# Kernel tuning notes

Measured on AMD Instinct MI355X. Metric: run time of the kernel, lower is better.

Reference implementation:

```python
import jax, jax.numpy as jnp
import numpy as np

NUM_EXPERTS = 8
TOP_K = 2
HIDDEN = 2048
INTER = 7168
B, S = 4, 2048


def setup_inputs() -> dict:
    key = jax.random.key(0)
    k0, k1, k2, k3, k4 = jax.random.split(key, 5)
    scale_h = 1.0 / np.sqrt(HIDDEN)
    scale_i = 1.0 / np.sqrt(INTER)
    return {
        "hidden_states": jax.random.normal(k0, (B, S, HIDDEN), dtype=jnp.float32),
        "gate_w": jax.random.normal(k1, (NUM_EXPERTS, HIDDEN), dtype=jnp.float32) * scale_h,
        "w1": jax.random.normal(k2, (NUM_EXPERTS, INTER, HIDDEN), dtype=jnp.float32) * scale_h,
        "w3": jax.random.normal(k3, (NUM_EXPERTS, INTER, HIDDEN), dtype=jnp.float32) * scale_h,
        "w2": jax.random.normal(k4, (NUM_EXPERTS, HIDDEN, INTER), dtype=jnp.float32) * scale_i,
    }


def reference(hidden_states, gate_w, w1, w3, w2):
    orig_shape = hidden_states.shape
    x = hidden_states.reshape(-1, HIDDEN)              # [T, H]

    # Router: gate linear -> softmax -> top-k -> renormalize.
    router_logits = x @ gate_w.T                       # [T, E]
    probs = jax.nn.softmax(router_logits, axis=-1)
    topk_w, topk_idx = jax.lax.top_k(probs, TOP_K)     # [T, K]
    topk_w = topk_w / jnp.sum(topk_w, axis=-1, keepdims=True)

    # Dense combine weights: [T, E] with top-k renormalized weights scattered.
    combine = jnp.sum(
        jax.nn.one_hot(topk_idx, NUM_EXPERTS, dtype=x.dtype) * topk_w[..., None],
        axis=1,
    )                                                   # [T, E]

    out = jnp.zeros_like(x)
    # Fixed small loop over experts (structurally distinct weight matrices);
    # avoids materializing a [T, E, I] intermediate.
    for e in range(NUM_EXPERTS):
        g = jax.nn.silu(x @ w1[e].T)                   # [T, I]
        u = x @ w3[e].T                                # [T, I]
        y = (g * u) @ w2[e].T                          # [T, H]
        out = out + combine[:, e:e + 1] * y

    return out.reshape(orig_shape)
```

## Files before the change

### kernel.cpp

```cpp
#include <hip/hip_runtime.h>
#include <stdint.h>

#define NE    8
#define HID   2048
#define INTER 7168
#define TTOK  8192
#define NT1   (HID / 64)
#define NT2   (INTER / 64)

typedef __bf16 bf16;
typedef bf16 bf16x4 __attribute__((ext_vector_type(4)));
typedef bf16 bf16x8 __attribute__((ext_vector_type(8)));
typedef float f32x4 __attribute__((ext_vector_type(4)));

__device__ __forceinline__ void glds16(const void* g, void* l) {
  __builtin_amdgcn_global_load_lds((__attribute__((address_space(1))) void*)g,
                                   (__attribute__((address_space(3))) void*)l, 16, 0, 0);
}

__global__ void cvt_f32_bf16(const float* __restrict__ src, bf16* __restrict__ dst, long n) {
  long i = (long)blockIdx.x * blockDim.x + threadIdx.x;
  long stride = (long)gridDim.x * blockDim.x;
  for (long j = i * 4; j < n; j += stride * 4) {
    float4 v = *(const float4*)(src + j);
    bf16x4 o = {(bf16)v.x, (bf16)v.y, (bf16)v.z, (bf16)v.w};
    *(bf16x4*)(dst + j) = o;
  }
}

__global__ void router_kernel(const float* __restrict__ x, const float* __restrict__ gw,
                              int* __restrict__ topk_e, float* __restrict__ topk_w) {
  const int wid = threadIdx.x >> 6, lane = threadIdx.x & 63;
  const int t = blockIdx.x * 4 + wid;
  if (t >= TTOK) return;
  const float* xr = x + (size_t)t * HID;
  float xv[32];
#pragma unroll
  for (int i = 0; i < 32; ++i) xv[i] = xr[lane + 64 * i];
  float lg[NE];
#pragma unroll
  for (int e = 0; e < NE; ++e) {
    const float* g = gw + e * HID;
    float s = 0.f;
#pragma unroll
    for (int i = 0; i < 32; ++i) s += xv[i] * g[lane + 64 * i];
#pragma unroll
    for (int off = 32; off; off >>= 1) s += __shfl_down(s, off);
    lg[e] = s;
  }
  if (lane == 0) {
    int i1 = 0;
#pragma unroll
    for (int e = 1; e < NE; ++e) if (lg[e] > lg[i1]) i1 = e;
    int i2 = (i1 == 0) ? 1 : 0;
#pragma unroll
    for (int e = 0; e < NE; ++e) if (e != i2 && e != i1 && lg[e] > lg[i2]) i2 = e;
    float r = __expf(lg[i2] - lg[i1]);
    float wa = 1.f / (1.f + r);
    topk_e[2 * t] = i1; topk_e[2 * t + 1] = i2;
    topk_w[2 * t] = wa; topk_w[2 * t + 1] = 1.f - wa;
  }
}

__global__ void gather_sorted(const int* __restrict__ topk_e, const float* __restrict__ topk_w,
                              int* __restrict__ cnt, int* __restrict__ ltok,
                              float* __restrict__ lw, int* __restrict__ ppos) {
  const int e = blockIdx.x;
  const int tid = threadIdx.x;
  const int lane = tid & 63, wv = tid >> 6;
  __shared__ int wtot[4];
  __shared__ int basesh;
  if (tid == 0) basesh = 0;
  __syncthreads();
  for (int c0 = 0; c0 < TTOK; c0 += 256) {
    const int t = c0 + tid;
    const int e0 = topk_e[2 * t], e1 = topk_e[2 * t + 1];
    const int j = (e0 == e) ? 0 : 1;
    const int flag = (e0 == e) || (e1 == e);
    unsigned long long b = __ballot(flag);
    int wrank = __popcll(b & ((1ULL << lane) - 1ULL));
    if (lane == 63) wtot[wv] = __popcll(b);
    __syncthreads();
    int wbase = 0;
#pragma unroll
    for (int k = 0; k < 4; ++k) if (k < wv) wbase += wtot[k];
    const int total = wtot[0] + wtot[1] + wtot[2] + wtot[3];
    const int pos = basesh + wbase + wrank;
    if (flag) {
      ltok[e * TTOK + pos] = t;
      lw[e * TTOK + pos] = (j == 0) ? topk_w[2 * t] : topk_w[2 * t + 1];
      ppos[2 * t + j] = pos;
    }
    __syncthreads();
    if (tid == 0) basesh += total;
    __syncthreads();
  }
  if (tid == 0) cnt[e] = basesh;
}

__global__ void prefix_kernel(const int* __restrict__ cnt, int* __restrict__ base) {
  if (threadIdx.x == 0 && blockIdx.x == 0) {
    int b = 0;
    for (int e = 0; e < NE; ++e) { base[e] = b; b += cnt[e]; }
    base[NE] = b;
  }
}

__global__ void combine_kernel(const float* __restrict__ ybuf, const int* __restrict__ topk_e,
                               const int* __restrict__ ppos, const int* __restrict__ basep,
                               float* __restrict__ out) {
  const int t = blockIdx.x;
  const int col = threadIdx.x * 8;
  const int g0 = basep[topk_e[2 * t]] + ppos[2 * t];
  const int g1 = basep[topk_e[2 * t + 1]] + ppos[2 * t + 1];
  const float4* y0 = (const float4*)(ybuf + (size_t)g0 * HID + col);
  const float4* y1 = (const float4*)(ybuf + (size_t)g1 * HID + col);
  float4* o = (float4*)(out + (size_t)t * HID + col);
  float4 a0 = y0[0], b0 = y1[0];
  float4 a1 = y0[1], b1 = y1[1];
  o[0] = make_float4(a0.x + b0.x, a0.y + b0.y, a0.z + b0.z, a0.w + b0.w);
  o[1] = make_float4(a1.x + b1.x, a1.y + b1.y, a1.z + b1.z, a1.w + b1.w);
}


#define MFMA(a, b, c) __builtin_amdgcn_mfma_f32_16x16x32_bf16((a), (b), (c), 0, 0, 0)

#define STAGE_A(h, kt) do { int _b = ((kt) & 1) * 32768; size_t _k = (size_t)(kt) * 128; \
    glds16(bA + oA[(h)*2 + 0] + _k, ldsA + _b + (h) * 16384 + d0); \
    glds16(bA + oA[(h)*2 + 1] + _k, ldsA + _b + (h) * 16384 + d1); } while (0)
#define STAGE_B(h, kt) do { int _b = ((kt) & 1) * 32768; size_t _k = (size_t)(kt) * 128; \
    glds16(bB + oB[(h)*2 + 0] + _k, ldsB + _b + (h) * 16384 + d0); \
    glds16(bB + oB[(h)*2 + 1] + _k, ldsB + _b + (h) * 16384 + d1); } while (0)

#define RD_A(mf, ks) (*(const bf16x8*)(ldsA + curb + arow + (mf) * (16 * 128) + ((ks) ? kcol1 : kcol0)))
#define RD_B(nf, ks) (*(const bf16x8*)(ldsB + curb + brow + (nf) * (16 * 128) + ((ks) ? kcol1 : kcol0)))

#define BAR()    __builtin_amdgcn_s_barrier()
#define LGKMC(n) do { asm volatile("s_waitcnt lgkmcnt(" #n ")" ::: "memory"); \
                      __builtin_amdgcn_sched_barrier(0); } while (0)
#define SCHED0() __builtin_amdgcn_sched_barrier(0)

#define Q_MFMA(AM, BM, ACCM, ACCN_OFF) do { \
  __builtin_amdgcn_s_setprio(1); \
  _Pragma("unroll") \
  for (int m = 0; m < 4; ++m) \
    _Pragma("unroll") \
    for (int n = 0; n < 2; ++n) { \
      acc[ACCM + m][ACCN_OFF + n] = MFMA(AM[m][0], BM[n][0], acc[ACCM + m][ACCN_OFF + n]); \
      acc[ACCM + m][ACCN_OFF + n] = MFMA(AM[m][1], BM[n][1], acc[ACCM + m][ACCN_OFF + n]); \
    } \
  __builtin_amdgcn_s_setprio(0); \
} while (0)

__launch_bounds__(512, 2)
__global__ void pass1_kernel(const bf16* __restrict__ xb, const bf16* __restrict__ w1b,
                             bf16* __restrict__ hbuf, const int* __restrict__ cnt,
                             const int* __restrict__ basep, const int* __restrict__ ltok) {
  const int e = blockIdx.z;
  const int c = cnt[e];
  const int tm = blockIdx.y;
  if (tm * 256 >= c) return;
  const int tn = blockIdx.x;

  __shared__ __align__(16) bf16 sA[2][256 * 64];
  __shared__ __align__(16) bf16 sB[2][256 * 64];
  char* const ldsA = (char*)&sA[0][0];
  char* const ldsB = (char*)&sB[0][0];

  const int tid = threadIdx.x;
  const int r0 = tid >> 3;
  const int ls = (tid & 7) ^ (r0 & 7);
  const int d0 = tid * 16, d1 = (tid + 512) * 16;
  const char* const bA = (const char*)xb;
  const char* const bB = (const char*)w1b;

  uint32_t oA[4], oB[4];
#pragma unroll
  for (int i = 0; i < 4; ++i) {
    int trow = i * 64 + r0;
    int slot = tm * 256 + trow; if (slot >= c) slot = c - 1;
    oA[i] = (uint32_t)((size_t)ltok[e * TTOK + slot] * (HID * 2) + ls * 16);
    int br = i * 64 + r0;
    int w = (br >> 4) & 1;
    int wr = tn * 128 + ((br >> 5) << 4) + (br & 15);
    size_t off = ((size_t)e * INTER + wr) * (HID * 2) + (size_t)ls * 16;
    if (w) off += (size_t)NE * INTER * HID * 2;
    oB[i] = (uint32_t)off;
  }

  const int lane = tid & 63, wid = tid >> 6;
  const int wm = wid >> 2, wn = wid & 3;
  const int ln15 = lane & 15, kq = lane >> 4;
  const int swz = (ln15 & 7) << 4;
  const int kcol0 = (kq * 16) ^ swz;
  const int kcol1 = (64 + kq * 16) ^ swz;
  const int arow = (wm * 128 + ln15) * 128;
  const int brow = (wn * 64 + ln15) * 128;

  f32x4 acc[8][4];
#pragma unroll
  for (int m = 0; m < 8; ++m)
#pragma unroll
    for (int n = 0; n < 4; ++n) acc[m][n] = (f32x4){0.f, 0.f, 0.f, 0.f};

  STAGE_A(0, 0); STAGE_A(1, 0); STAGE_B(0, 0); STAGE_B(1, 0);
  asm volatile("s_waitcnt vmcnt(4)" ::: "memory");
  STAGE_A(0, 1); STAGE_A(1, 1); STAGE_B(0, 1);
  asm volatile("s_waitcnt vmcnt(6)" ::: "memory");
  BAR();

  bf16x8 a0[4][2], a1[4][2], b0[2][2], b1[2][2];
  int cur = 0;
  for (int t = 0; t < NT1; ++t, cur ^= 1) {
    const int curb = cur * 32768;
#pragma unroll
    for (int m = 0; m < 4; ++m) { a0[m][0] = RD_A(m, 0); a0[m][1] = RD_A(m, 1); }
#pragma unroll
    for (int n = 0; n < 2; ++n) { b0[n][0] = RD_B(n, 0); b0[n][1] = RD_B(n, 1); }
    if (t + 1 < NT1) STAGE_B(1, t + 1);
    BAR(); LGKMC(12);
    if (t > 0) Q_MFMA(a1, b1, 4, 2);
    BAR();
#pragma unroll
    for (int m = 0; m < 4; ++m) { a1[m][0] = RD_A(4 + m, 0); a1[m][1] = RD_A(4 + m, 1); }
    BAR(); LGKMC(8);
    Q_MFMA(a0, b0, 0, 0);
    BAR();
#pragma unroll
    for (int n = 0; n < 2; ++n) { b1[n][0] = RD_B(2 + n, 0); b1[n][1] = RD_B(2 + n, 1); }
    if (t + 2 < NT1) { STAGE_A(0, t + 2); STAGE_A(1, t + 2); SCHED0(); }
    BAR(); LGKMC(4);
    Q_MFMA(a1, b0, 4, 0);
    BAR();
    if (t + 2 < NT1) STAGE_B(0, t + 2);
    LGKMC(0);
    Q_MFMA(a0, b1, 0, 2);
    if (t + 2 < NT1) asm volatile("s_waitcnt vmcnt(6)" ::: "memory");
    else             asm volatile("s_waitcnt vmcnt(0)" ::: "memory");
    BAR();
  }
  Q_MFMA(a1, b1, 4, 2);

  const int be = basep[e];
#pragma unroll
  for (int mh = 0; mh < 2; ++mh)
#pragma unroll
    for (int mf = 0; mf < 4; ++mf)
#pragma unroll
      for (int j = 0; j < 4; ++j) {
        const int slot = tm * 256 + wm * 128 + mh * 64 + mf * 16 + kq * 4 + j;
        if (slot < c) {
          bf16* hrow = hbuf + (size_t)(be + slot) * INTER + tn * 128;
#pragma unroll
          for (int p = 0; p < 2; ++p) {
            const float g = acc[mh * 4 + mf][2 * p][j];
            const float u = acc[mh * 4 + mf][2 * p + 1][j];
            const float hv = g / (1.f + __expf(-g)) * u;
            hrow[wn * 32 + p * 16 + ln15] = (bf16)hv;
          }
        }
      }
}

__launch_bounds__(512, 2)
__global__ void pass2_kernel(const bf16* __restrict__ hbuf, const bf16* __restrict__ w2b,
                             float* __restrict__ ybuf, const int* __restrict__ cnt,
                             const int* __restrict__ basep, const float* __restrict__ lw) {
  const int e = blockIdx.z;
  const int c = cnt[e];
  const int tm = blockIdx.y;
  if (tm * 256 >= c) return;
  const int tn = blockIdx.x;

  __shared__ __align__(16) bf16 sA[2][256 * 64];
  __shared__ __align__(16) bf16 sB[2][256 * 64];
  char* const ldsA = (char*)&sA[0][0];
  char* const ldsB = (char*)&sB[0][0];

  const int tid = threadIdx.x;
  const int r0 = tid >> 3;
  const int ls = (tid & 7) ^ (r0 & 7);
  const int d0 = tid * 16, d1 = (tid + 512) * 16;
  const int be = basep[e];
  const char* const bA = (const char*)hbuf;
  const char* const bB = (const char*)w2b;

  uint32_t oA[4], oB[4];
#pragma unroll
  for (int i = 0; i < 4; ++i) {
    int trow = i * 64 + r0;
    int slot = tm * 256 + trow; if (slot >= c) slot = c - 1;
    oA[i] = (uint32_t)((size_t)(be + slot) * (INTER * 2) + ls * 16);
    oB[i] = (uint32_t)(((size_t)e * HID + tn * 256 + i * 64 + r0) * (INTER * 2) + (size_t)ls * 16);
  }

  const int lane = tid & 63, wid = tid >> 6;
  const int wm = wid >> 2, wn = wid & 3;
  const int ln15 = lane & 15, kq = lane >> 4;
  const int swz = (ln15 & 7) << 4;
  const int kcol0 = (kq * 16) ^ swz;
  const int kcol1 = (64 + kq * 16) ^ swz;
  const int arow = (wm * 128 + ln15) * 128;
  const int brow = (wn * 64 + ln15) * 128;

  f32x4 acc[8][4];
#pragma unroll
  for (int m = 0; m < 8; ++m)
#pragma unroll
    for (int n = 0; n < 4; ++n) acc[m][n] = (f32x4){0.f, 0.f, 0.f, 0.f};

  STAGE_A(0, 0); STAGE_A(1, 0); STAGE_B(0, 0); STAGE_B(1, 0);
  asm volatile("s_waitcnt vmcnt(4)" ::: "memory");
  STAGE_A(0, 1); STAGE_A(1, 1); STAGE_B(0, 1);
  asm volatile("s_waitcnt vmcnt(6)" ::: "memory");
  BAR();

  bf16x8 a0[4][2], a1[4][2], b0[2][2], b1[2][2];
  int cur = 0;
  for (int t = 0; t < NT2; ++t, cur ^= 1) {
    const int curb = cur * 32768;
#pragma unroll
    for (int m = 0; m < 4; ++m) { a0[m][0] = RD_A(m, 0); a0[m][1] = RD_A(m, 1); }
#pragma unroll
    for (int n = 0; n < 2; ++n) { b0[n][0] = RD_B(n, 0); b0[n][1] = RD_B(n, 1); }
    if (t + 1 < NT2) STAGE_B(1, t + 1);
    BAR(); LGKMC(12);
    if (t > 0) Q_MFMA(a1, b1, 4, 2);
    BAR();
#pragma unroll
    for (int m = 0; m < 4; ++m) { a1[m][0] = RD_A(4 + m, 0); a1[m][1] = RD_A(4 + m, 1); }
    BAR(); LGKMC(8);
    Q_MFMA(a0, b0, 0, 0);
    BAR();
#pragma unroll
    for (int n = 0; n < 2; ++n) { b1[n][0] = RD_B(2 + n, 0); b1[n][1] = RD_B(2 + n, 1); }
    if (t + 2 < NT2) { STAGE_A(0, t + 2); STAGE_A(1, t + 2); SCHED0(); }
    BAR(); LGKMC(4);
    Q_MFMA(a1, b0, 4, 0);
    BAR();
    if (t + 2 < NT2) STAGE_B(0, t + 2);
    LGKMC(0);
    Q_MFMA(a0, b1, 0, 2);
    if (t + 2 < NT2) asm volatile("s_waitcnt vmcnt(6)" ::: "memory");
    else             asm volatile("s_waitcnt vmcnt(0)" ::: "memory");
    BAR();
  }
  Q_MFMA(a1, b1, 4, 2);

#pragma unroll
  for (int mh = 0; mh < 2; ++mh)
#pragma unroll
    for (int mf = 0; mf < 4; ++mf)
#pragma unroll
      for (int j = 0; j < 4; ++j) {
        const int slot = tm * 256 + wm * 128 + mh * 64 + mf * 16 + kq * 4 + j;
        if (slot < c) {
          const float wt = lw[e * TTOK + slot];
          float* yrow = ybuf + (size_t)(be + slot) * HID + tn * 256;
#pragma unroll
          for (int n = 0; n < 4; ++n)
            yrow[wn * 64 + n * 16 + ln15] = wt * acc[mh * 4 + mf][n][j];
        }
      }
}

extern "C" void kernel_launch(void* const* d_in, const int* in_sizes, int n_in,
                              void* d_out, int out_size, void* d_ws, size_t ws_size,
                              hipStream_t stream) {
  const float* x  = (const float*)d_in[0];
  const float* gw = (const float*)d_in[1];
  const float* w1 = (const float*)d_in[2];
  const float* w3 = (const float*)d_in[3];
  const float* w2 = (const float*)d_in[4];
  float* out = (float*)d_out;

  char* ws = (char*)d_ws;
  size_t off = 0;
  auto take = [&](size_t bytes) -> char* {
    char* p = ws + off;
    off += (bytes + 255) & ~(size_t)255;
    return p;
  };
  bf16* xb    = (bf16*)take((size_t)TTOK * HID * 2);
  bf16* w1b   = (bf16*)take((size_t)NE * INTER * HID * 2);
  bf16* w3b   = (bf16*)take((size_t)NE * INTER * HID * 2);
  bf16* w2b   = (bf16*)take((size_t)NE * HID * INTER * 2);
  bf16* hbuf  = (bf16*)take((size_t)TTOK * 2 * INTER * 2);
  float* ybuf = (float*)take((size_t)TTOK * 2 * HID * 4);
  int*   topk_e = (int*)take(TTOK * 2 * 4);
  float* topk_w = (float*)take(TTOK * 2 * 4);
  int*   ltok   = (int*)take(NE * TTOK * 4);
  float* lwgt   = (float*)take(NE * TTOK * 4);
  int*   ppos   = (int*)take(TTOK * 2 * 4);
  int*   cntp   = (int*)take(64);
  int*   basep  = (int*)take(64);
  if (off > ws_size) return;

  cvt_f32_bf16<<<2048, 256, 0, stream>>>(x,  xb,  (long)TTOK * HID);
  cvt_f32_bf16<<<4096, 256, 0, stream>>>(w1, w1b, (long)NE * INTER * HID);
  cvt_f32_bf16<<<4096, 256, 0, stream>>>(w3, w3b, (long)NE * INTER * HID);
  cvt_f32_bf16<<<4096, 256, 0, stream>>>(w2, w2b, (long)NE * HID * INTER);

  router_kernel<<<TTOK / 4, 256, 0, stream>>>(x, gw, topk_e, topk_w);
  gather_sorted<<<NE, 256, 0, stream>>>(topk_e, topk_w, cntp, ltok, lwgt, ppos);
  prefix_kernel<<<1, 64, 0, stream>>>(cntp, basep);

  pass1_kernel<<<dim3(INTER / 128, TTOK / 256, NE), 512, 0, stream>>>(
      xb, w1b, hbuf, cntp, basep, ltok);
  pass2_kernel<<<dim3(HID / 256, TTOK / 256, NE), 512, 0, stream>>>(
      hbuf, w2b, ybuf, cntp, basep, lwgt);
  combine_kernel<<<TTOK, 256, 0, stream>>>(ybuf, topk_e, ppos, basep, out);
}
```

Baseline: 2.103 ms.

## Fuse fp32-to-bf16 weight conversion into GEMM B-tile loads

Removes the three separate weight conversion kernels and has pass1/pass2 load fp32 weights straight into registers, convert them to bf16 and write them to LDS. This drops the full-size bf16 weight write and re-read (about 1.4 GB of fp32 read plus bf16 write/read). In exchange, each GEMM tile now re-reads fp32 weights, twice the bytes per load, and does so once per token tile, with register staging in place of async direct-to-LDS loads. That can add global traffic and register pressure in the main loop.

```diff
diff --git a/kernel.cpp b/kernel.cpp
--- a/kernel.cpp
+++ b/kernel.cpp
@@ -16,6 +16,13 @@
 __device__ __forceinline__ void glds16(const void* g, void* l) {
   __builtin_amdgcn_global_load_lds((__attribute__((address_space(1))) void*)g,
                                    (__attribute__((address_space(3))) void*)l, 16, 0, 0);
+}
+
+__device__ __forceinline__ bf16x8 cvt8(float4 lo, float4 hi) {
+  bf16x8 v;
+  v[0] = (bf16)lo.x; v[1] = (bf16)lo.y; v[2] = (bf16)lo.z; v[3] = (bf16)lo.w;
+  v[4] = (bf16)hi.x; v[5] = (bf16)hi.y; v[6] = (bf16)hi.z; v[7] = (bf16)hi.w;
+  return v;
 }
 
 __global__ void cvt_f32_bf16(const float* __restrict__ src, bf16* __restrict__ dst, long n) {
@@ -128,9 +135,19 @@
 #define STAGE_A(h, kt) do { int _b = ((kt) & 1) * 32768; size_t _k = (size_t)(kt) * 128; \
     glds16(bA + oA[(h)*2 + 0] + _k, ldsA + _b + (h) * 16384 + d0); \
     glds16(bA + oA[(h)*2 + 1] + _k, ldsA + _b + (h) * 16384 + d1); } while (0)
-#define STAGE_B(h, kt) do { int _b = ((kt) & 1) * 32768; size_t _k = (size_t)(kt) * 128; \
-    glds16(bB + oB[(h)*2 + 0] + _k, ldsB + _b + (h) * 16384 + d0); \
-    glds16(bB + oB[(h)*2 + 1] + _k, ldsB + _b + (h) * 16384 + d1); } while (0)
+
+#define BLOAD(kt) do { size_t _k = (size_t)(kt) * 256; \
+    _Pragma("unroll") \
+    for (int i = 0; i < 4; ++i) { \
+      bl[i][0] = *(const float4*)(pB + oBf[i] + _k); \
+      bl[i][1] = *(const float4*)(pB + oBf[i] + _k + 16); \
+    } } while (0)
+
+#define BWRITE(kt) do { int _nb = ((kt) & 1) * 32768; \
+    _Pragma("unroll") \
+    for (int i = 0; i < 4; ++i) { \
+      *(bf16x8*)(ldsB + _nb + (i >> 1) * 16384 + ((i & 1) ? d1 : d0)) = cvt8(bl[i][0], bl[i][1]); \
+    } } while (0)
 
 #define RD_A(mf, ks) (*(const bf16x8*)(ldsA + curb + arow + (mf) * (16 * 128) + ((ks) ? kcol1 : kcol0)))
 #define RD_B(nf, ks) (*(const bf16x8*)(ldsB + curb + brow + (nf) * (16 * 128) + ((ks) ? kcol1 : kcol0)))
@@ -138,6 +155,7 @@
 #define BAR()    __builtin_amdgcn_s_barrier()
 #define LGKMC(n) do { asm volatile("s_waitcnt lgkmcnt(" #n ")" ::: "memory"); \
                       __builtin_amdgcn_sched_barrier(0); } while (0)
+#define VMC(n)   asm volatile("s_waitcnt vmcnt(" #n ")" ::: "memory")
 #define SCHED0() __builtin_amdgcn_sched_barrier(0)
 
 #define Q_MFMA(AM, BM, ACCM, ACCN_OFF) do { \
@@ -153,9 +171,10 @@
 } while (0)
 
 __launch_bounds__(512, 2)
-__global__ void pass1_kernel(const bf16* __restrict__ xb, const bf16* __restrict__ w1b,
-                             bf16* __restrict__ hbuf, const int* __restrict__ cnt,
-                             const int* __restrict__ basep, const int* __restrict__ ltok) {
+__global__ void pass1_kernel(const bf16* __restrict__ xb, const float* __restrict__ w1f,
+                             const float* __restrict__ w3f, bf16* __restrict__ hbuf,
+                             const int* __restrict__ cnt, const int* __restrict__ basep,
+                             const int* __restrict__ ltok) {
   const int e = blockIdx.z;
   const int c = cnt[e];
   const int tm = blockIdx.y;
@@ -172,20 +191,15 @@
   const int ls = (tid & 7) ^ (r0 & 7);
   const int d0 = tid * 16, d1 = (tid + 512) * 16;
   const char* const bA = (const char*)xb;
-  const char* const bB = (const char*)w1b;
-
-  uint32_t oA[4], oB[4];
+  const char* const pB = (const char*)(((r0 >> 4) & 1) ? w3f : w1f);
+
+  uint32_t oA[4], oBf[4];
 #pragma unroll
   for (int i = 0; i < 4; ++i) {
-    int trow = i * 64 + r0;
-    int slot = tm * 256 + trow; if (slot >= c) slot = c - 1;
+    int slot = tm * 256 + i * 64 + r0; if (slot >= c) slot = c - 1;
     oA[i] = (uint32_t)((size_t)ltok[e * TTOK + slot] * (HID * 2) + ls * 16);
-    int br = i * 64 + r0;
-    int w = (br >> 4) & 1;
-    int wr = tn * 128 + ((br >> 5) << 4) + (br & 15);
-    size_t off = ((size_t)e * INTER + wr) * (HID * 2) + (size_t)ls * 16;
-    if (w) off += (size_t)NE * INTER * HID * 2;
-    oB[i] = (uint32_t)off;
+    int wr = tn * 128 + ((i * 2 + (r0 >> 5)) << 4) + (r0 & 15);
+    oBf[i] = (uint32_t)(((size_t)(e * INTER + wr) * HID + ls * 8) * 4);
   }
 
   const int lane = tid & 63, wid = tid >> 6;
@@ -203,10 +217,14 @@
 #pragma unroll
     for (int n = 0; n < 4; ++n) acc[m][n] = (f32x4){0.f, 0.f, 0.f, 0.f};
 
-  STAGE_A(0, 0); STAGE_A(1, 0); STAGE_B(0, 0); STAGE_B(1, 0);
-  asm volatile("s_waitcnt vmcnt(4)" ::: "memory");
-  STAGE_A(0, 1); STAGE_A(1, 1); STAGE_B(0, 1);
-  asm volatile("s_waitcnt vmcnt(6)" ::: "memory");
+  float4 bl[4][2];
+  BLOAD(0); SCHED0();
+  STAGE_A(0, 0); STAGE_A(1, 0);
+  STAGE_A(0, 1); STAGE_A(1, 1);
+  VMC(8);
+  BWRITE(0);
+  VMC(4);
+  LGKMC(0);
   BAR();
 
   bf16x8 a0[4][2], a1[4][2], b0[2][2], b1[2][2];
@@ -217,7 +235,7 @@
     for (int m = 0; m < 4; ++m) { a0[m][0] = RD_A(m, 0); a0[m][1] = RD_A(m, 1); }
 #pragma unroll
     for (int n = 0; n < 2; ++n) { b0[n][0] = RD_B(n, 0); b0[n][1] = RD_B(n, 1); }
-    if (t + 1 < NT1) STAGE_B(1, t + 1);
+    if (t + 1 < NT1) { BLOAD(t + 1); SCHED0(); }
     BAR(); LGKMC(12);
     if (t > 0) Q_MFMA(a1, b1, 4, 2);
     BAR();
@@ -232,11 +250,11 @@
     BAR(); LGKMC(4);
     Q_MFMA(a1, b0, 4, 0);
     BAR();
-    if (t + 2 < NT1) STAGE_B(0, t + 2);
+    if (t + 2 < NT1) VMC(4);
+    else             VMC(0);
+    if (t + 1 < NT1) BWRITE(t + 1);
     LGKMC(0);
     Q_MFMA(a0, b1, 0, 2);
-    if (t + 2 < NT1) asm volatile("s_waitcnt vmcnt(6)" ::: "memory");
-    else             asm volatile("s_waitcnt vmcnt(0)" ::: "memory");
     BAR();
   }
   Q_MFMA(a1, b1, 4, 2);
@@ -263,7 +281,7 @@
 }
 
 __launch_bounds__(512, 2)
-__global__ void pass2_kernel(const bf16* __restrict__ hbuf, const bf16* __restrict__ w2b,
+__global__ void pass2_kernel(const bf16* __restrict__ hbuf, const float* __restrict__ w2f,
                              float* __restrict__ ybuf, const int* __restrict__ cnt,
                              const int* __restrict__ basep, const float* __restrict__ lw) {
   const int e = blockIdx.z;
@@ -283,15 +301,14 @@
   const int d0 = tid * 16, d1 = (tid + 512) * 16;
   const int be = basep[e];
   const char* const bA = (const char*)hbuf;
-  const char* const bB = (const char*)w2b;
-
-  uint32_t oA[4], oB[4];
+  const char* const pB = (const char*)w2f;
+
+  uint32_t oA[4], oBf[4];
 #pragma unroll
   for (int i = 0; i < 4; ++i) {
-    int trow = i * 64 + r0;
-    int slot = tm * 256 + trow; if (slot >= c) slot = c - 1;
+    int slot = tm * 256 + i * 64 + r0; if (slot >= c) slot = c - 1;
     oA[i] = (uint32_t)((size_t)(be + slot) * (INTER * 2) + ls * 16);
-    oB[i] = (uint32_t)(((size_t)e * HID + tn * 256 + i * 64 + r0) * (INTER * 2) + (size_t)ls * 16);
+    oBf[i] = (uint32_t)(((size_t)(e * HID + tn * 256 + i * 64 + r0) * INTER + ls * 8) * 4);
   }
 
   const int lane = tid & 63, wid = tid >> 6;
@@ -309,10 +326,14 @@
 #pragma unroll
     for (int n = 0; n < 4; ++n) acc[m][n] = (f32x4){0.f, 0.f, 0.f, 0.f};
 
-  STAGE_A(0, 0); STAGE_A(1, 0); STAGE_B(0, 0); STAGE_B(1, 0);
-  asm volatile("s_waitcnt vmcnt(4)" ::: "memory");
-  STAGE_A(0, 1); STAGE_A(1, 1); STAGE_B(0, 1);
-  asm volatile("s_waitcnt vmcnt(6)" ::: "memory");
+  float4 bl[4][2];
+  BLOAD(0); SCHED0();
+  STAGE_A(0, 0); STAGE_A(1, 0);
+  STAGE_A(0, 1); STAGE_A(1, 1);
+  VMC(8);
+  BWRITE(0);
+  VMC(4);
+  LGKMC(0);
   BAR();
 
   bf16x8 a0[4][2], a1[4][2], b0[2][2], b1[2][2];
@@ -323,7 +344,7 @@
     for (int m = 0; m < 4; ++m) { a0[m][0] = RD_A(m, 0); a0[m][1] = RD_A(m, 1); }
 #pragma unroll
     for (int n = 0; n < 2; ++n) { b0[n][0] = RD_B(n, 0); b0[n][1] = RD_B(n, 1); }
-    if (t + 1 < NT2) STAGE_B(1, t + 1);
+    if (t + 1 < NT2) { BLOAD(t + 1); SCHED0(); }
     BAR(); LGKMC(12);
     if (t > 0) Q_MFMA(a1, b1, 4, 2);
     BAR();
@@ -338,11 +359,11 @@
     BAR(); LGKMC(4);
     Q_MFMA(a1, b0, 4, 0);
     BAR();
-    if (t + 2 < NT2) STAGE_B(0, t + 2);
+    if (t + 2 < NT2) VMC(4);
+    else             VMC(0);
+    if (t + 1 < NT2) BWRITE(t + 1);
     LGKMC(0);
     Q_MFMA(a0, b1, 0, 2);
-    if (t + 2 < NT2) asm volatile("s_waitcnt vmcnt(6)" ::: "memory");
-    else             asm volatile("s_waitcnt vmcnt(0)" ::: "memory");
     BAR();
   }
   Q_MFMA(a1, b1, 4, 2);
@@ -382,9 +403,6 @@
     return p;
   };
   bf16* xb    = (bf16*)take((size_t)TTOK * HID * 2);
-  bf16* w1b   = (bf16*)take((size_t)NE * INTER * HID * 2);
-  bf16* w3b   = (bf16*)take((size_t)NE * INTER * HID * 2);
-  bf16* w2b   = (bf16*)take((size_t)NE * HID * INTER * 2);
   bf16* hbuf  = (bf16*)take((size_t)TTOK * 2 * INTER * 2);
   float* ybuf = (float*)take((size_t)TTOK * 2 * HID * 4);
   int*   topk_e = (int*)take(TTOK * 2 * 4);
@@ -396,18 +414,15 @@
   int*   basep  = (int*)take(64);
   if (off > ws_size) return;
 
-  cvt_f32_bf16<<<2048, 256, 0, stream>>>(x,  xb,  (long)TTOK * HID);
-  cvt_f32_bf16<<<4096, 256, 0, stream>>>(w1, w1b, (long)NE * INTER * HID);
-  cvt_f32_bf16<<<4096, 256, 0, stream>>>(w3, w3b, (long)NE * INTER * HID);
-  cvt_f32_bf16<<<4096, 256, 0, stream>>>(w2, w2b, (long)NE * HID * INTER);
+  cvt_f32_bf16<<<2048, 256, 0, stream>>>(x, xb, (long)TTOK * HID);
 
   router_kernel<<<TTOK / 4, 256, 0, stream>>>(x, gw, topk_e, topk_w);
   gather_sorted<<<NE, 256, 0, stream>>>(topk_e, topk_w, cntp, ltok, lwgt, ppos);
   prefix_kernel<<<1, 64, 0, stream>>>(cntp, basep);
 
   pass1_kernel<<<dim3(INTER / 128, TTOK / 256, NE), 512, 0, stream>>>(
-      xb, w1b, hbuf, cntp, basep, ltok);
+      xb, w1, w3, hbuf, cntp, basep, ltok);
   pass2_kernel<<<dim3(HID / 256, TTOK / 256, NE), 512, 0, stream>>>(
-      hbuf, w2b, ybuf, cntp, basep, lwgt);
+      hbuf, w2, ybuf, cntp, basep, lwgt);
   combine_kernel<<<TTOK, 256, 0, stream>>>(ybuf, topk_e, ppos, basep, out);
 }
```

New measurement: 4.865 ms. 131% more time.

## Fuse x conversion into router and overlap w2 conversion with pass1

Applied to the files above, without the earlier changes.

The router now writes the bf16 copy of x while it already holds the row in registers, which removes a separate conversion kernel and one extra read of x. The w2 fp32-to-bf16 conversion is moved into an extra z-slice of the pass1 grid, so it runs alongside the expert GEMM blocks instead of as its own launch. This saves launches and lets the memory-bound conversion overlap compute, at the cost of the conversion blocks competing with GEMM blocks for CU slots and bandwidth.

```diff
diff --git a/kernel.cpp b/kernel.cpp
--- a/kernel.cpp
+++ b/kernel.cpp
@@ -29,14 +29,18 @@
 }
 
 __global__ void router_kernel(const float* __restrict__ x, const float* __restrict__ gw,
+                              bf16* __restrict__ xb,
                               int* __restrict__ topk_e, float* __restrict__ topk_w) {
   const int wid = threadIdx.x >> 6, lane = threadIdx.x & 63;
   const int t = blockIdx.x * 4 + wid;
   if (t >= TTOK) return;
   const float* xr = x + (size_t)t * HID;
+  bf16* xw = xb + (size_t)t * HID;
   float xv[32];
 #pragma unroll
   for (int i = 0; i < 32; ++i) xv[i] = xr[lane + 64 * i];
+#pragma unroll
+  for (int i = 0; i < 32; ++i) xw[lane + 64 * i] = (bf16)xv[i];
   float lg[NE];
 #pragma unroll
   for (int e = 0; e < NE; ++e) {
@@ -154,9 +158,23 @@
 
 __launch_bounds__(512, 2)
 __global__ void pass1_kernel(const bf16* __restrict__ xb, const bf16* __restrict__ w1b,
+                             const float* __restrict__ w2f, bf16* __restrict__ w2b,
                              bf16* __restrict__ hbuf, const int* __restrict__ cnt,
                              const int* __restrict__ basep, const int* __restrict__ ltok) {
-  const int e = blockIdx.z;
+  if (blockIdx.z == 0) {
+    const long n4 = (long)NE * HID * INTER / 4;
+    long i = (long)(blockIdx.y * gridDim.x + blockIdx.x) * blockDim.x + threadIdx.x;
+    const long stride = (long)gridDim.x * gridDim.y * blockDim.x;
+    const float4* src = (const float4*)w2f;
+    bf16x4* dst = (bf16x4*)w2b;
+    for (long j = i; j < n4; j += stride) {
+      float4 v = src[j];
+      bf16x4 o = {(bf16)v.x, (bf16)v.y, (bf16)v.z, (bf16)v.w};
+      dst[j] = o;
+    }
+    return;
+  }
+  const int e = blockIdx.z - 1;
   const int c = cnt[e];
   const int tm = blockIdx.y;
   if (tm * 256 >= c) return;
@@ -177,8 +195,7 @@
   uint32_t oA[4], oB[4];
 #pragma unroll
   for (int i = 0; i < 4; ++i) {
-    int trow = i * 64 + r0;
-    int slot = tm * 256 + trow; if (slot >= c) slot = c - 1;
+    int slot = tm * 256 + i * 64 + r0; if (slot >= c) slot = c - 1;
     oA[i] = (uint32_t)((size_t)ltok[e * TTOK + slot] * (HID * 2) + ls * 16);
     int br = i * 64 + r0;
     int w = (br >> 4) & 1;
@@ -288,8 +305,7 @@
   uint32_t oA[4], oB[4];
 #pragma unroll
   for (int i = 0; i < 4; ++i) {
-    int trow = i * 64 + r0;
-    int slot = tm * 256 + trow; if (slot >= c) slot = c - 1;
+    int slot = tm * 256 + i * 64 + r0; if (slot >= c) slot = c - 1;
     oA[i] = (uint32_t)((size_t)(be + slot) * (INTER * 2) + ls * 16);
     oB[i] = (uint32_t)(((size_t)e * HID + tn * 256 + i * 64 + r0) * (INTER * 2) + (size_t)ls * 16);
   }
@@ -396,17 +412,15 @@
   int*   basep  = (int*)take(64);
   if (off > ws_size) return;
 
-  cvt_f32_bf16<<<2048, 256, 0, stream>>>(x,  xb,  (long)TTOK * HID);
   cvt_f32_bf16<<<4096, 256, 0, stream>>>(w1, w1b, (long)NE * INTER * HID);
   cvt_f32_bf16<<<4096, 256, 0, stream>>>(w3, w3b, (long)NE * INTER * HID);
-  cvt_f32_bf16<<<4096, 256, 0, stream>>>(w2, w2b, (long)NE * HID * INTER);
-
-  router_kernel<<<TTOK / 4, 256, 0, stream>>>(x, gw, topk_e, topk_w);
+
+  router_kernel<<<TTOK / 4, 256, 0, stream>>>(x, gw, xb, topk_e, topk_w);
   gather_sorted<<<NE, 256, 0, stream>>>(topk_e, topk_w, cntp, ltok, lwgt, ppos);
   prefix_kernel<<<1, 64, 0, stream>>>(cntp, basep);
 
-  pass1_kernel<<<dim3(INTER / 128, TTOK / 256, NE), 512, 0, stream>>>(
-      xb, w1b, hbuf, cntp, basep, ltok);
+  pass1_kernel<<<dim3(INTER / 128, TTOK / 256, NE + 1), 512, 0, stream>>>(
+      xb, w1b, w2, w2b, hbuf, cntp, basep, ltok);
   pass2_kernel<<<dim3(HID / 256, TTOK / 256, NE), 512, 0, stream>>>(
       hbuf, w2b, ybuf, cntp, basep, lwgt);
   combine_kernel<<<TTOK, 256, 0, stream>>>(ybuf, topk_e, ppos, basep, out);
```

Result: no change. 2.121 ms (+0.8%).
